# Performance work log

Hardware: AMD Instinct MI355X
Metric: run time of the kernel (lower is better)

Reference implementation:

```python
import jax, jax.numpy as jnp
import numpy as np

B, CL, QL, D = 32, 1024, 512, 256


def setup_inputs() -> dict:
    key = jax.random.key(0)
    ks = jax.random.split(key, 8)
    c = jax.random.normal(ks[0], (B, CL, D), jnp.float32)
    q = jax.random.normal(ks[1], (B, QL, D), jnp.float32)
    scale = 1.0 / np.sqrt(D)
    w_c = jax.random.normal(ks[2], (D,), jnp.float32) * scale
    b_c = jax.random.normal(ks[3], (), jnp.float32) * 0.01
    w_q = jax.random.normal(ks[4], (D,), jnp.float32) * scale
    b_q = jax.random.normal(ks[5], (), jnp.float32) * 0.01
    w_cq = jax.random.normal(ks[6], (D,), jnp.float32) * scale
    b_cq = jax.random.normal(ks[7], (), jnp.float32) * 0.01
    return {"c": c, "q": q, "w_c": w_c, "b_c": b_c, "w_q": w_q, "b_q": b_q,
            "w_cq": w_cq, "b_cq": b_cq}


def reference(c, q, w_c, b_c, w_q, b_q, w_cq, b_cq):
    # s[b,i,j] = w_c.c_i + w_q.q_j + w_cq.(c_i*q_j) + biases
    sc = c @ w_c + b_c                                   # (B, CL)
    sq = q @ w_q + b_q                                   # (B, QL)
    # The original per-j loop att_weight_cq(c * q_j) is a batched bilinear form.
    cq = jnp.einsum('bid,bjd,d->bij', c, q, w_cq) + b_cq  # (B, CL, QL)
    s = sc[:, :, None] + sq[:, None, :] + cq              # (B, CL, QL)
    a = jax.nn.softmax(s, axis=2)
    c2q_att = jnp.einsum('bij,bjd->bid', a, q)            # (B, CL, D)
    bvec = jax.nn.softmax(jnp.max(s, axis=2), axis=1)     # (B, CL)
    q2c = jnp.einsum('bi,bid->bd', bvec, c)               # (B, D)
    q2c_att = jnp.broadcast_to(q2c[:, None, :], c.shape)  # (B, CL, D)
    x = jnp.concatenate([c, c2q_att, c * c2q_att, c * q2c_att], axis=-1)
    return x
```

## Files before the change

### kernel.cpp

```cpp
#include <hip/hip_runtime.h>

#define B_  32
#define CL_ 1024
#define QL_ 512
#define D_  256

typedef _Float16 f16;
typedef __attribute__((ext_vector_type(2))) _Float16 f16x2;
typedef __attribute__((ext_vector_type(4))) _Float16 f16x4;
typedef __attribute__((ext_vector_type(8))) _Float16 f16x8;
typedef __attribute__((ext_vector_type(4))) float    f32x4;

__global__ __launch_bounds__(256) void k0_prep(const float* __restrict__ q,
                                               const float* __restrict__ w_q,
                                               f16* __restrict__ q_h,
                                               f16* __restrict__ qT_h,
                                               float* __restrict__ sqv) {
  __shared__ f16 q_l[64][258];
  int b = blockIdx.y, j0 = blockIdx.x * 64, tid = threadIdx.x;
  int r = tid >> 2, seg = tid & 3;
  const float* qrow = q   + ((size_t)(b * QL_ + j0 + r)) * D_ + seg * 64;
  f16*        qhrow = q_h + ((size_t)(b * QL_ + j0 + r)) * D_ + seg * 64;
  float dot = 0.f;
  #pragma unroll
  for (int u = 0; u < 16; ++u) {
    f32x4 v  = *(const f32x4*)(qrow + 4 * u);
    f32x4 wv = *(const f32x4*)(w_q + seg * 64 + 4 * u);
    f16x4 h;
    h[0] = (f16)v[0]; h[1] = (f16)v[1]; h[2] = (f16)v[2]; h[3] = (f16)v[3];
    *(f16x4*)(&q_l[r][seg * 64 + 4 * u]) = h;
    *(f16x4*)(qhrow + 4 * u) = h;
    dot += v[0]*wv[0] + v[1]*wv[1] + v[2]*wv[2] + v[3]*wv[3];
  }
  dot += __shfl_xor(dot, 1, 64);
  dot += __shfl_xor(dot, 2, 64);
  if (seg == 0) sqv[b * QL_ + j0 + r] = dot;
  __syncthreads();
  f16* qTb = qT_h + (size_t)b * D_ * QL_ + j0;
  #pragma unroll
  for (int s = 0; s < 32; ++s) {
    int e = tid + 256 * s;
    int d = e >> 5, j2 = (e & 31) * 2;
    f16x2 p;
    p[0] = q_l[j2][d];
    p[1] = q_l[j2 + 1][d];
    *(f16x2*)(qTb + (size_t)d * QL_ + j2) = p;
  }
}

__global__ __launch_bounds__(512, 4) void k1_fused(
    const float* __restrict__ c, const f16* __restrict__ q_h,
    const f16* __restrict__ qT_h, const float* __restrict__ sqv,
    const float* __restrict__ w_c, const float* __restrict__ w_cq,
    float* __restrict__ out, float* __restrict__ mrow)
{
  __shared__ alignas(16) char smem[73472];
  f16 (*cw_t)[264]  = (f16 (*)[264])(smem);
  f16 (*P_t)[520]   = (f16 (*)[520])(smem);
  float (*o_l)[260] = (float (*)[260])(smem);
  float* sqv_l = (float*)(smem + 66560);
  float* wcq_l = (float*)(smem + 68608);
  float* wc_l  = (float*)(smem + 69632);
  float* scv_l = (float*)(smem + 70656);
  float (*red)[64] = (float (*)[64])(smem + 70912);
  float* mf = (float*)(smem + 72960);
  float* lf = (float*)(smem + 73216);

  const int tid = threadIdx.x;
  const int w = tid >> 6, l = tid & 63, g = l >> 4, l15 = l & 15;
  const int lin = blockIdx.x, xcd = lin & 7, slot = lin >> 3;
  const int b  = xcd * 4 + (slot >> 4);
  const int i0 = (slot & 15) * 64;

  if (tid < 256) { wcq_l[tid] = w_cq[tid]; wc_l[tid] = w_c[tid]; }
  sqv_l[tid] = sqv[b * QL_ + tid];
  __syncthreads();

  {
    int row = tid >> 3, seg = tid & 7;
    const float* crow = c + (size_t)(b * CL_ + i0 + row) * D_ + seg * 32;
    float dot = 0.f;
    #pragma unroll
    for (int u = 0; u < 8; ++u) {
      f32x4 v  = *(const f32x4*)(crow + 4 * u);
      f32x4 wv = *(const f32x4*)(wcq_l + seg * 32 + 4 * u);
      f32x4 w2 = *(const f32x4*)(wc_l  + seg * 32 + 4 * u);
      f16x4 h;
      h[0] = (f16)(v[0]*wv[0]); h[1] = (f16)(v[1]*wv[1]);
      h[2] = (f16)(v[2]*wv[2]); h[3] = (f16)(v[3]*wv[3]);
      *(f16x4*)(&cw_t[row][seg * 32 + 4 * u]) = h;
      dot += v[0]*w2[0] + v[1]*w2[1] + v[2]*w2[2] + v[3]*w2[3];
    }
    dot += __shfl_xor(dot, 1, 64); dot += __shfl_xor(dot, 2, 64);
    dot += __shfl_xor(dot, 4, 64);
    if (seg == 0) scv_l[row] = dot;
  }
  __syncthreads();

  f32x4 acc[4][4];
  #pragma unroll
  for (int fi = 0; fi < 4; ++fi)
    #pragma unroll
    for (int fj = 0; fj < 4; ++fj)
      acc[fi][fj] = (f32x4){0.f,0.f,0.f,0.f};

  const f16* qb = q_h + (size_t)b * QL_ * D_ + (size_t)(64 * w + l15) * D_ + 8 * g;
  #pragma unroll
  for (int dk = 0; dk < 8; ++dk) {
    f16x8 av[4];
    #pragma unroll
    for (int fi = 0; fi < 4; ++fi)
      av[fi] = *(const f16x8*)(&cw_t[16 * fi + l15][dk * 32 + 8 * g]);
    #pragma unroll
    for (int fj = 0; fj < 4; ++fj) {
      f16x8 bf = *(const f16x8*)(qb + (size_t)(16 * fj) * D_ + dk * 32);
      #pragma unroll
      for (int fi = 0; fi < 4; ++fi)
        acc[fi][fj] = __builtin_amdgcn_mfma_f32_16x16x32_f16(av[fi], bf, acc[fi][fj], 0, 0, 0);
    }
  }

  #pragma unroll
  for (int fi = 0; fi < 4; ++fi) {
    #pragma unroll
    for (int r = 0; r < 4; ++r) {
      float mx = -1e30f;
      #pragma unroll
      for (int fj = 0; fj < 4; ++fj) {
        float v = acc[fi][fj][r] + sqv_l[64 * w + 16 * fj + l15];
        acc[fi][fj][r] = v;
        mx = fmaxf(mx, v);
      }
      mx = fmaxf(mx, __shfl_xor(mx, 1, 64));
      mx = fmaxf(mx, __shfl_xor(mx, 2, 64));
      mx = fmaxf(mx, __shfl_xor(mx, 4, 64));
      mx = fmaxf(mx, __shfl_xor(mx, 8, 64));
      if (l15 == 0) red[w][16 * fi + 4 * g + r] = mx;
    }
  }
  __syncthreads();
  if (tid < 64) {
    float m = red[0][tid];
    #pragma unroll
    for (int w2 = 1; w2 < 8; ++w2) m = fmaxf(m, red[w2][tid]);
    mf[tid] = m;
    mrow[b * CL_ + i0 + tid] = m + scv_l[tid];
  }
  __syncthreads();
  #pragma unroll
  for (int fi = 0; fi < 4; ++fi) {
    #pragma unroll
    for (int r = 0; r < 4; ++r) {
      float mv = mf[16 * fi + 4 * g + r];
      float s = 0.f;
      #pragma unroll
      for (int fj = 0; fj < 4; ++fj) {
        float p = __expf(acc[fi][fj][r] - mv);
        acc[fi][fj][r] = p;
        s += p;
      }
      s += __shfl_xor(s, 1, 64); s += __shfl_xor(s, 2, 64);
      s += __shfl_xor(s, 4, 64); s += __shfl_xor(s, 8, 64);
      if (l15 == 0) red[w][16 * fi + 4 * g + r] = s;
    }
  }
  __syncthreads();
  if (tid < 64) {
    float s = 0.f;
    #pragma unroll
    for (int w2 = 0; w2 < 8; ++w2) s += red[w2][tid];
    lf[tid] = 1.0f / s;
  }
  __syncthreads();

  #pragma unroll
  for (int fi = 0; fi < 4; ++fi) {
    #pragma unroll
    for (int r = 0; r < 4; ++r) {
      int row = 16 * fi + 4 * g + r;
      float inv = lf[row];
      #pragma unroll
      for (int fj = 0; fj < 4; ++fj)
        P_t[row][64 * w + 16 * fj + l15] = (f16)(acc[fi][fj][r] * inv);
    }
  }
  __syncthreads();

  f32x4 o[4][2];
  #pragma unroll
  for (int fi = 0; fi < 4; ++fi) { o[fi][0] = (f32x4){0.f,0.f,0.f,0.f}; o[fi][1] = o[fi][0]; }
  const f16* qTb = qT_h + (size_t)b * D_ * QL_ + (size_t)(32 * w + l15) * QL_ + 8 * g;
  #pragma unroll
  for (int jt = 0; jt < 16; ++jt) {
    f16x8 qf0 = *(const f16x8*)(qTb + jt * 32);
    f16x8 qf1 = *(const f16x8*)(qTb + 16 * QL_ + jt * 32);
    #pragma unroll
    for (int fi = 0; fi < 4; ++fi) {
      f16x8 pa = *(const f16x8*)(&P_t[16 * fi + l15][jt * 32 + 8 * g]);
      o[fi][0] = __builtin_amdgcn_mfma_f32_16x16x32_f16(pa, qf0, o[fi][0], 0, 0, 0);
      o[fi][1] = __builtin_amdgcn_mfma_f32_16x16x32_f16(pa, qf1, o[fi][1], 0, 0, 0);
    }
  }
  __syncthreads();

  #pragma unroll
  for (int fi = 0; fi < 4; ++fi)
    #pragma unroll
    for (int fd = 0; fd < 2; ++fd)
      #pragma unroll
      for (int r = 0; r < 4; ++r)
        o_l[16 * fi + 4 * g + r][32 * w + 16 * fd + l15] = o[fi][fd][r];
  __syncthreads();

  #pragma unroll
  for (int s = 0; s < 8; ++s) {
    int idx = tid + 512 * s;
    int row = idx >> 6, c4 = (idx & 63) * 4;
    size_t rowoff = (size_t)(b * CL_ + i0 + row);
    f32x4 c2q = *(const f32x4*)(&o_l[row][c4]);
    f32x4 cv  = *(const f32x4*)(c + rowoff * D_ + c4);
    f32x4 prod;
    prod[0] = cv[0]*c2q[0]; prod[1] = cv[1]*c2q[1];
    prod[2] = cv[2]*c2q[2]; prod[3] = cv[3]*c2q[3];
    float* ob = out + rowoff * (4 * D_) + c4;
    *(f32x4*)(ob)          = cv;
    *(f32x4*)(ob + D_)     = c2q;
    *(f32x4*)(ob + 2 * D_) = prod;
  }
}

__global__ __launch_bounds__(256) void k2a_bvec(const float* __restrict__ mrow,
                                                float* __restrict__ bvec) {
  __shared__ float red[256];
  int b = blockIdx.x, tid = threadIdx.x;
  f32x4 v = *(const f32x4*)(mrow + b * CL_ + tid * 4);
  float mx = fmaxf(fmaxf(v[0], v[1]), fmaxf(v[2], v[3]));
  red[tid] = mx;
  __syncthreads();
  for (int s = 128; s > 0; s >>= 1) {
    if (tid < s) red[tid] = fmaxf(red[tid], red[tid + s]);
    __syncthreads();
  }
  float gmx = red[0];
  __syncthreads();
  f32x4 e;
  e[0] = __expf(v[0] - gmx); e[1] = __expf(v[1] - gmx);
  e[2] = __expf(v[2] - gmx); e[3] = __expf(v[3] - gmx);
  red[tid] = e[0] + e[1] + e[2] + e[3];
  __syncthreads();
  for (int s = 128; s > 0; s >>= 1) {
    if (tid < s) red[tid] += red[tid + s];
    __syncthreads();
  }
  float inv = 1.0f / red[0];
  e[0] *= inv; e[1] *= inv; e[2] *= inv; e[3] *= inv;
  *(f32x4*)(bvec + b * CL_ + tid * 4) = e;
}

__global__ __launch_bounds__(256) void k2b_part(const float* __restrict__ c,
                                                const float* __restrict__ bvec,
                                                float* __restrict__ part) {
  __shared__ f32x4 pl[4][64];
  int ch = blockIdx.x, b = blockIdx.y, tid = threadIdx.x;
  int ro = tid >> 6, dl = tid & 63;
  const float* cb = c + ((size_t)b * CL_ + ch * 128) * D_;
  const float* bv = bvec + b * CL_ + ch * 128;
  f32x4 acc = (f32x4){0.f, 0.f, 0.f, 0.f};
  for (int i = ro; i < 128; i += 4) {
    float wgt = bv[i];
    f32x4 v = *(const f32x4*)(cb + (size_t)i * D_ + dl * 4);
    acc[0] += wgt * v[0]; acc[1] += wgt * v[1];
    acc[2] += wgt * v[2]; acc[3] += wgt * v[3];
  }
  pl[ro][dl] = acc;
  __syncthreads();
  if (tid < 64) {
    f32x4 s = (pl[0][tid] + pl[1][tid]) + (pl[2][tid] + pl[3][tid]);
    *(f32x4*)(part + ((size_t)(b * 8 + ch)) * D_ + tid * 4) = s;
  }
}

__global__ __launch_bounds__(256) void k2c_red(const float* __restrict__ part,
                                               float* __restrict__ q2c) {
  int b = blockIdx.x, d = threadIdx.x;
  float s = 0.f;
  #pragma unroll
  for (int ch = 0; ch < 8; ++ch) s += part[((size_t)(b * 8 + ch)) * D_ + d];
  q2c[b * D_ + d] = s;
}

__global__ __launch_bounds__(256) void k3_tail(const float* __restrict__ c,
                                               const float* __restrict__ q2c,
                                               float* __restrict__ out) {
  size_t idx = (size_t)blockIdx.x * 256 + threadIdx.x;
  int b   = (int)(idx >> 16);
  int rem = (int)(idx & 65535);
  int i = rem >> 6, d4 = (rem & 63) * 4;
  f32x4 cv = *(const f32x4*)(c + (size_t)(b * CL_ + i) * D_ + d4);
  f32x4 gv = *(const f32x4*)(q2c + b * D_ + d4);
  f32x4 r;
  r[0] = cv[0]*gv[0]; r[1] = cv[1]*gv[1]; r[2] = cv[2]*gv[2]; r[3] = cv[3]*gv[3];
  *(f32x4*)(out + (size_t)(b * CL_ + i) * (4 * D_) + 3 * D_ + d4) = r;
}

extern "C" void kernel_launch(void* const* d_in, const int* in_sizes, int n_in,
                              void* d_out, int out_size, void* d_ws, size_t ws_size,
                              hipStream_t stream) {
  const float* c    = (const float*)d_in[0];
  const float* q    = (const float*)d_in[1];
  const float* w_c  = (const float*)d_in[2];
  const float* w_q  = (const float*)d_in[4];
  const float* w_cq = (const float*)d_in[6];
  float* out = (float*)d_out;
  char* ws = (char*)d_ws;
  f16*   q_h  = (f16*)ws;
  f16*   qT_h = (f16*)(ws + 8388608);
  float* sqv  = (float*)(ws + 16777216);
  float* mrow = (float*)(ws + 16842752);
  float* bvec = (float*)(ws + 16973824);
  float* part = (float*)(ws + 17104896);
  float* q2c  = (float*)(ws + 17367040);

  hipLaunchKernelGGL(k0_prep,  dim3(8, 32),  dim3(256), 0, stream,
                     q, w_q, q_h, qT_h, sqv);
  hipLaunchKernelGGL(k1_fused, dim3(512),    dim3(512), 0, stream,
                     c, q_h, qT_h, sqv, w_c, w_cq, out, mrow);
  hipLaunchKernelGGL(k2a_bvec, dim3(32),     dim3(256), 0, stream, mrow, bvec);
  hipLaunchKernelGGL(k2b_part, dim3(8, 32),  dim3(256), 0, stream, c, bvec, part);
  hipLaunchKernelGGL(k2c_red,  dim3(32),     dim3(256), 0, stream, part, q2c);
  hipLaunchKernelGGL(k3_tail,  dim3(8192),   dim3(256), 0, stream, c, q2c, out);
}
```

Measured before the change: 101.2 us.

## Split fused attention kernel into scores, softmax and PV GEMM kernels

Replaces the single fused kernel with three kernels. The first computes the scores and writes them to a global f16 buffer. The second applies the row softmax in place and records row maxima. The third runs a finer-tiled PV GEMM with smaller blocks and writes the output slices. The intent is to raise occupancy and parallelism of the PV stage and to shorten the long fused kernel. In exchange it adds large global round-trips of the score matrix, extra launches, and f16 rounding of the scores before the softmax.

Result: slower. 146.1 us (+44.4%).

```diff
diff --git a/kernel.cpp b/kernel.cpp
--- a/kernel.cpp
+++ b/kernel.cpp
@@ -48,23 +48,18 @@
   }
 }
 
-__global__ __launch_bounds__(512, 4) void k1_fused(
+__global__ __launch_bounds__(512, 2) void kU_scores(
     const float* __restrict__ c, const f16* __restrict__ q_h,
-    const f16* __restrict__ qT_h, const float* __restrict__ sqv,
-    const float* __restrict__ w_c, const float* __restrict__ w_cq,
-    float* __restrict__ out, float* __restrict__ mrow)
+    const float* __restrict__ sqv, const float* __restrict__ w_c,
+    const float* __restrict__ w_cq, f16* __restrict__ Ug,
+    float* __restrict__ scv_ws)
 {
-  __shared__ alignas(16) char smem[73472];
-  f16 (*cw_t)[264]  = (f16 (*)[264])(smem);
-  f16 (*P_t)[520]   = (f16 (*)[520])(smem);
-  float (*o_l)[260] = (float (*)[260])(smem);
+  __shared__ alignas(16) char smem[71680];
+  f16 (*cw_t)[264] = (f16 (*)[264])(smem);
+  f16 (*U_t)[520]  = (f16 (*)[520])(smem);
   float* sqv_l = (float*)(smem + 66560);
   float* wcq_l = (float*)(smem + 68608);
   float* wc_l  = (float*)(smem + 69632);
-  float* scv_l = (float*)(smem + 70656);
-  float (*red)[64] = (float (*)[64])(smem + 70912);
-  float* mf = (float*)(smem + 72960);
-  float* lf = (float*)(smem + 73216);
 
   const int tid = threadIdx.x;
   const int w = tid >> 6, l = tid & 63, g = l >> 4, l15 = l & 15;
@@ -93,7 +88,7 @@
     }
     dot += __shfl_xor(dot, 1, 64); dot += __shfl_xor(dot, 2, 64);
     dot += __shfl_xor(dot, 4, 64);
-    if (seg == 0) scv_l[row] = dot;
+    if (seg == 0) scv_ws[b * CL_ + i0 + row] = dot;
   }
   __syncthreads();
 
@@ -119,110 +114,113 @@
         acc[fi][fj] = __builtin_amdgcn_mfma_f32_16x16x32_f16(av[fi], bf, acc[fi][fj], 0, 0, 0);
     }
   }
-
-  #pragma unroll
-  for (int fi = 0; fi < 4; ++fi) {
+  __syncthreads();
+
+  #pragma unroll
+  for (int fi = 0; fi < 4; ++fi)
     #pragma unroll
     for (int r = 0; r < 4; ++r) {
-      float mx = -1e30f;
+      int row = 16 * fi + 4 * g + r;
       #pragma unroll
       for (int fj = 0; fj < 4; ++fj) {
-        float v = acc[fi][fj][r] + sqv_l[64 * w + 16 * fj + l15];
-        acc[fi][fj][r] = v;
-        mx = fmaxf(mx, v);
+        int col = 64 * w + 16 * fj + l15;
+        U_t[row][col] = (f16)(acc[fi][fj][r] + sqv_l[col]);
       }
-      mx = fmaxf(mx, __shfl_xor(mx, 1, 64));
-      mx = fmaxf(mx, __shfl_xor(mx, 2, 64));
-      mx = fmaxf(mx, __shfl_xor(mx, 4, 64));
-      mx = fmaxf(mx, __shfl_xor(mx, 8, 64));
-      if (l15 == 0) red[w][16 * fi + 4 * g + r] = mx;
     }
-  }
-  __syncthreads();
-  if (tid < 64) {
-    float m = red[0][tid];
-    #pragma unroll
-    for (int w2 = 1; w2 < 8; ++w2) m = fmaxf(m, red[w2][tid]);
-    mf[tid] = m;
-    mrow[b * CL_ + i0 + tid] = m + scv_l[tid];
-  }
-  __syncthreads();
-  #pragma unroll
-  for (int fi = 0; fi < 4; ++fi) {
-    #pragma unroll
-    for (int r = 0; r < 4; ++r) {
-      float mv = mf[16 * fi + 4 * g + r];
-      float s = 0.f;
-      #pragma unroll
-      for (int fj = 0; fj < 4; ++fj) {
-        float p = __expf(acc[fi][fj][r] - mv);
-        acc[fi][fj][r] = p;
-        s += p;
-      }
-      s += __shfl_xor(s, 1, 64); s += __shfl_xor(s, 2, 64);
-      s += __shfl_xor(s, 4, 64); s += __shfl_xor(s, 8, 64);
-      if (l15 == 0) red[w][16 * fi + 4 * g + r] = s;
-    }
-  }
-  __syncthreads();
-  if (tid < 64) {
-    float s = 0.f;
-    #pragma unroll
-    for (int w2 = 0; w2 < 8; ++w2) s += red[w2][tid];
-    lf[tid] = 1.0f / s;
-  }
-  __syncthreads();
-
-  #pragma unroll
-  for (int fi = 0; fi < 4; ++fi) {
-    #pragma unroll
-    for (int r = 0; r < 4; ++r) {
-      int row = 16 * fi + 4 * g + r;
-      float inv = lf[row];
-      #pragma unroll
-      for (int fj = 0; fj < 4; ++fj)
-        P_t[row][64 * w + 16 * fj + l15] = (f16)(acc[fi][fj][r] * inv);
-    }
-  }
-  __syncthreads();
-
-  f32x4 o[4][2];
-  #pragma unroll
-  for (int fi = 0; fi < 4; ++fi) { o[fi][0] = (f32x4){0.f,0.f,0.f,0.f}; o[fi][1] = o[fi][0]; }
-  const f16* qTb = qT_h + (size_t)b * D_ * QL_ + (size_t)(32 * w + l15) * QL_ + 8 * g;
-  #pragma unroll
-  for (int jt = 0; jt < 16; ++jt) {
-    f16x8 qf0 = *(const f16x8*)(qTb + jt * 32);
-    f16x8 qf1 = *(const f16x8*)(qTb + 16 * QL_ + jt * 32);
-    #pragma unroll
-    for (int fi = 0; fi < 4; ++fi) {
-      f16x8 pa = *(const f16x8*)(&P_t[16 * fi + l15][jt * 32 + 8 * g]);
-      o[fi][0] = __builtin_amdgcn_mfma_f32_16x16x32_f16(pa, qf0, o[fi][0], 0, 0, 0);
-      o[fi][1] = __builtin_amdgcn_mfma_f32_16x16x32_f16(pa, qf1, o[fi][1], 0, 0, 0);
-    }
-  }
-  __syncthreads();
-
-  #pragma unroll
-  for (int fi = 0; fi < 4; ++fi)
+  __syncthreads();
+
+  f16* Ub = Ug + ((size_t)(b * CL_ + i0)) * QL_;
+  #pragma unroll
+  for (int s = 0; s < 8; ++s) {
+    int idx = tid + 512 * s;
+    int row = idx >> 6, col8 = (idx & 63) * 8;
+    *(f16x8*)(Ub + (size_t)row * QL_ + col8) = *(const f16x8*)(&U_t[row][col8]);
+  }
+}
+
+__global__ __launch_bounds__(256) void kSM_softmax(
+    f16* __restrict__ UPg, const float* __restrict__ scv_ws,
+    float* __restrict__ mrow)
+{
+  int gr   = blockIdx.x * 4 + (threadIdx.x >> 6);
+  int lane = threadIdx.x & 63;
+  f16* rp = UPg + (size_t)gr * QL_ + lane * 8;
+  f16x8 uv = *(const f16x8*)rp;
+  float u[8];
+  #pragma unroll
+  for (int k = 0; k < 8; ++k) u[k] = (float)uv[k];
+  float mx = u[0];
+  #pragma unroll
+  for (int k = 1; k < 8; ++k) mx = fmaxf(mx, u[k]);
+  #pragma unroll
+  for (int m = 1; m < 64; m <<= 1) mx = fmaxf(mx, __shfl_xor(mx, m, 64));
+  if (lane == 0) mrow[gr] = mx + scv_ws[gr];
+  float s = 0.f;
+  #pragma unroll
+  for (int k = 0; k < 8; ++k) { u[k] = __expf(u[k] - mx); s += u[k]; }
+  #pragma unroll
+  for (int m = 1; m < 64; m <<= 1) s += __shfl_xor(s, m, 64);
+  float inv = 1.0f / s;
+  f16x8 pv;
+  #pragma unroll
+  for (int k = 0; k < 8; ++k) pv[k] = (f16)(u[k] * inv);
+  *(f16x8*)rp = pv;
+}
+
+__global__ __launch_bounds__(256, 4) void kPV_gemm(
+    const float* __restrict__ c, const f16* __restrict__ Pg,
+    const f16* __restrict__ qT_h, float* __restrict__ out)
+{
+  __shared__ float o_l[64][68];
+  const int tid = threadIdx.x;
+  const int w = tid >> 6, l = tid & 63, g = l >> 4, l15 = l & 15;
+  const int lin = blockIdx.x, xcd = lin & 7, slot = lin >> 3;
+  const int b   = xcd * 4 + (slot >> 6);
+  const int rem = slot & 63;
+  const int i0 = (rem >> 2) * 64, d0 = (rem & 3) * 64;
+  const int wi = w >> 1, wd = w & 1;
+
+  const f16* a0p = Pg + ((size_t)(b * CL_ + i0 + 32 * wi + l15)) * QL_ + 8 * g;
+  const f16* a1p = a0p + 16 * QL_;
+  const f16* b0p = qT_h + (size_t)b * D_ * QL_
+                 + (size_t)(d0 + 32 * wd + l15) * QL_ + 8 * g;
+  const f16* b1p = b0p + 16 * QL_;
+
+  f32x4 acc[2][2];
+  acc[0][0] = (f32x4){0.f,0.f,0.f,0.f}; acc[0][1] = acc[0][0];
+  acc[1][0] = acc[0][0];                acc[1][1] = acc[0][0];
+  #pragma unroll
+  for (int kt = 0; kt < 16; ++kt) {
+    f16x8 a0 = *(const f16x8*)(a0p + kt * 32);
+    f16x8 a1 = *(const f16x8*)(a1p + kt * 32);
+    f16x8 b0 = *(const f16x8*)(b0p + kt * 32);
+    f16x8 b1 = *(const f16x8*)(b1p + kt * 32);
+    acc[0][0] = __builtin_amdgcn_mfma_f32_16x16x32_f16(a0, b0, acc[0][0], 0, 0, 0);
+    acc[0][1] = __builtin_amdgcn_mfma_f32_16x16x32_f16(a0, b1, acc[0][1], 0, 0, 0);
+    acc[1][0] = __builtin_amdgcn_mfma_f32_16x16x32_f16(a1, b0, acc[1][0], 0, 0, 0);
+    acc[1][1] = __builtin_amdgcn_mfma_f32_16x16x32_f16(a1, b1, acc[1][1], 0, 0, 0);
+  }
+
+  #pragma unroll
+  for (int fi = 0; fi < 2; ++fi)
     #pragma unroll
     for (int fd = 0; fd < 2; ++fd)
       #pragma unroll
       for (int r = 0; r < 4; ++r)
-        o_l[16 * fi + 4 * g + r][32 * w + 16 * fd + l15] = o[fi][fd][r];
-  __syncthreads();
-
-  #pragma unroll
-  for (int s = 0; s < 8; ++s) {
-    int idx = tid + 512 * s;
-    int row = idx >> 6, c4 = (idx & 63) * 4;
+        o_l[32 * wi + 16 * fi + 4 * g + r][32 * wd + 16 * fd + l15] = acc[fi][fd][r];
+  __syncthreads();
+
+  #pragma unroll
+  for (int s = 0; s < 4; ++s) {
+    int chunk = tid + 256 * s;
+    int row = chunk >> 4, col = (chunk & 15) * 4;
     size_t rowoff = (size_t)(b * CL_ + i0 + row);
-    f32x4 c2q = *(const f32x4*)(&o_l[row][c4]);
-    f32x4 cv  = *(const f32x4*)(c + rowoff * D_ + c4);
+    f32x4 c2q = *(const f32x4*)(&o_l[row][col]);
+    f32x4 cv  = *(const f32x4*)(c + rowoff * D_ + d0 + col);
     f32x4 prod;
     prod[0] = cv[0]*c2q[0]; prod[1] = cv[1]*c2q[1];
     prod[2] = cv[2]*c2q[2]; prod[3] = cv[3]*c2q[3];
-    float* ob = out + rowoff * (4 * D_) + c4;
+    float* ob = out + rowoff * (4 * D_) + d0 + col;
     *(f32x4*)(ob)          = cv;
     *(f32x4*)(ob + D_)     = c2q;
     *(f32x4*)(ob + 2 * D_) = prod;
@@ -313,20 +311,26 @@
   const float* w_cq = (const float*)d_in[6];
   float* out = (float*)d_out;
   char* ws = (char*)d_ws;
-  f16*   q_h  = (f16*)ws;
-  f16*   qT_h = (f16*)(ws + 8388608);
-  float* sqv  = (float*)(ws + 16777216);
-  float* mrow = (float*)(ws + 16842752);
-  float* bvec = (float*)(ws + 16973824);
-  float* part = (float*)(ws + 17104896);
-  float* q2c  = (float*)(ws + 17367040);
-
-  hipLaunchKernelGGL(k0_prep,  dim3(8, 32),  dim3(256), 0, stream,
+  f16*   q_h    = (f16*)ws;
+  f16*   qT_h   = (f16*)(ws + 8388608);
+  float* sqv    = (float*)(ws + 16777216);
+  float* mrow   = (float*)(ws + 16842752);
+  float* bvec   = (float*)(ws + 16973824);
+  float* part   = (float*)(ws + 17104896);
+  float* q2c    = (float*)(ws + 17367040);
+  float* scv_ws = (float*)(ws + 17399808);
+  f16*   UPg    = (f16*)(ws + 17530880);
+
+  hipLaunchKernelGGL(k0_prep,    dim3(8, 32),  dim3(256), 0, stream,
                      q, w_q, q_h, qT_h, sqv);
-  hipLaunchKernelGGL(k1_fused, dim3(512),    dim3(512), 0, stream,
-                     c, q_h, qT_h, sqv, w_c, w_cq, out, mrow);
-  hipLaunchKernelGGL(k2a_bvec, dim3(32),     dim3(256), 0, stream, mrow, bvec);
-  hipLaunchKernelGGL(k2b_part, dim3(8, 32),  dim3(256), 0, stream, c, bvec, part);
-  hipLaunchKernelGGL(k2c_red,  dim3(32),     dim3(256), 0, stream, part, q2c);
-  hipLaunchKernelGGL(k3_tail,  dim3(8192),   dim3(256), 0, stream, c, q2c, out);
-}
+  hipLaunchKernelGGL(kU_scores,  dim3(512),    dim3(512), 0, stream,
+                     c, q_h, sqv, w_c, w_cq, UPg, scv_ws);
+  hipLaunchKernelGGL(kSM_softmax,dim3(8192),   dim3(256), 0, stream,
+                     UPg, scv_ws, mrow);
+  hipLaunchKernelGGL(kPV_gemm,   dim3(2048),   dim3(256), 0, stream,
+                     c, UPg, qT_h, out);
+  hipLaunchKernelGGL(k2a_bvec,   dim3(32),     dim3(256), 0, stream, mrow, bvec);
+  hipLaunchKernelGGL(k2b_part,   dim3(8, 32),  dim3(256), 0, stream, c, bvec, part);
+  hipLaunchKernelGGL(k2c_red,    dim3(32),     dim3(256), 0, stream, part, q2c);
+  hipLaunchKernelGGL(k3_tail,    dim3(8192),   dim3(256), 0, stream, c, q2c, out);
+}
```

## Stage q and qT tiles through swizzled LDS for both GEMMs

Applied to the files above, without the earlier changes.

Replaces per-wave direct global loads of q and q-transpose fragments with cooperative block-wide loads into XOR-swizzled shared-memory tiles. The first GEMM is restructured into four j-chunks, and the second into four staged j-chunks. The goal is coalesced global reads and cheaper LDS-fed MFMA operands in place of strided 16-byte global loads. In exchange, LDS grows to about 136 KB, which cuts blocks per CU (the occupancy hint is dropped) and adds extra barriers per chunk.

New measurement: 178.6 us. 76.4% more time.

```diff
diff --git a/kernel.cpp b/kernel.cpp
--- a/kernel.cpp
+++ b/kernel.cpp
@@ -48,23 +48,25 @@
   }
 }
 
-__global__ __launch_bounds__(512, 4) void k1_fused(
+__global__ __launch_bounds__(512) void k1_fused(
     const float* __restrict__ c, const f16* __restrict__ q_h,
     const f16* __restrict__ qT_h, const float* __restrict__ sqv,
     const float* __restrict__ w_c, const float* __restrict__ w_cq,
     float* __restrict__ out, float* __restrict__ mrow)
 {
-  __shared__ alignas(16) char smem[73472];
+  __shared__ alignas(16) char smem[139008];
   f16 (*cw_t)[264]  = (f16 (*)[264])(smem);
+  char* qA          = smem + 34816;
   f16 (*P_t)[520]   = (f16 (*)[520])(smem);
+  char* qT          = smem + 66560;
   float (*o_l)[260] = (float (*)[260])(smem);
-  float* sqv_l = (float*)(smem + 66560);
-  float* wcq_l = (float*)(smem + 68608);
-  float* wc_l  = (float*)(smem + 69632);
-  float* scv_l = (float*)(smem + 70656);
-  float (*red)[64] = (float (*)[64])(smem + 70912);
-  float* mf = (float*)(smem + 72960);
-  float* lf = (float*)(smem + 73216);
+  float* sqv_l = (float*)(smem + 132096);
+  float* wcq_l = (float*)(smem + 134144);
+  float* wc_l  = (float*)(smem + 135168);
+  float* scv_l = (float*)(smem + 136192);
+  float (*red)[64] = (float (*)[64])(smem + 136448);
+  float* mf = (float*)(smem + 138496);
+  float* lf = (float*)(smem + 138752);
 
   const int tid = threadIdx.x;
   const int w = tid >> 6, l = tid & 63, g = l >> 4, l15 = l & 15;
@@ -95,29 +97,38 @@
     dot += __shfl_xor(dot, 4, 64);
     if (seg == 0) scv_l[row] = dot;
   }
-  __syncthreads();
 
   f32x4 acc[4][4];
   #pragma unroll
-  for (int fi = 0; fi < 4; ++fi)
-    #pragma unroll
-    for (int fj = 0; fj < 4; ++fj)
-      acc[fi][fj] = (f32x4){0.f,0.f,0.f,0.f};
-
-  const f16* qb = q_h + (size_t)b * QL_ * D_ + (size_t)(64 * w + l15) * D_ + 8 * g;
-  #pragma unroll
-  for (int dk = 0; dk < 8; ++dk) {
-    f16x8 av[4];
+  for (int jc = 0; jc < 4; ++jc)
     #pragma unroll
     for (int fi = 0; fi < 4; ++fi)
-      av[fi] = *(const f16x8*)(&cw_t[16 * fi + l15][dk * 32 + 8 * g]);
-    #pragma unroll
-    for (int fj = 0; fj < 4; ++fj) {
-      f16x8 bf = *(const f16x8*)(qb + (size_t)(16 * fj) * D_ + dk * 32);
-      #pragma unroll
-      for (int fi = 0; fi < 4; ++fi)
-        acc[fi][fj] = __builtin_amdgcn_mfma_f32_16x16x32_f16(av[fi], bf, acc[fi][fj], 0, 0, 0);
-    }
+      acc[jc][fi] = (f32x4){0.f,0.f,0.f,0.f};
+
+  const char* qhbC = (const char*)(q_h + (size_t)b * QL_ * D_);
+  const int jrow = 16 * w + l15;
+  const int jsw  = jrow & 7;
+  #pragma unroll 1
+  for (int jc = 0; jc < 4; ++jc) {
+    const char* src = qhbC + (size_t)jc * 65536;
+    #pragma unroll
+    for (int s = 0; s < 8; ++s) {
+      int idx = s * 512 + tid;
+      int row = idx >> 5, sl = idx & 31;
+      f32x4 v = *(const f32x4*)(src + (size_t)idx * 16);
+      *(f32x4*)(qA + row * 512 + ((sl ^ (row & 7)) << 4)) = v;
+    }
+    __syncthreads();
+    #pragma unroll
+    for (int dk = 0; dk < 8; ++dk) {
+      f16x8 bf = *(const f16x8*)(qA + jrow * 512 + (((dk * 4 + g) ^ jsw) << 4));
+      #pragma unroll
+      for (int fi = 0; fi < 4; ++fi) {
+        f16x8 av = *(const f16x8*)(&cw_t[16 * fi + l15][dk * 32 + 8 * g]);
+        acc[jc][fi] = __builtin_amdgcn_mfma_f32_16x16x32_f16(av, bf, acc[jc][fi], 0, 0, 0);
+      }
+    }
+    __syncthreads();
   }
 
   #pragma unroll
@@ -126,9 +137,9 @@
     for (int r = 0; r < 4; ++r) {
       float mx = -1e30f;
       #pragma unroll
-      for (int fj = 0; fj < 4; ++fj) {
-        float v = acc[fi][fj][r] + sqv_l[64 * w + 16 * fj + l15];
-        acc[fi][fj][r] = v;
+      for (int jc = 0; jc < 4; ++jc) {
+        float v = acc[jc][fi][r] + sqv_l[jc * 128 + jrow];
+        acc[jc][fi][r] = v;
         mx = fmaxf(mx, v);
       }
       mx = fmaxf(mx, __shfl_xor(mx, 1, 64));
@@ -154,9 +165,9 @@
       float mv = mf[16 * fi + 4 * g + r];
       float s = 0.f;
       #pragma unroll
-      for (int fj = 0; fj < 4; ++fj) {
-        float p = __expf(acc[fi][fj][r] - mv);
-        acc[fi][fj][r] = p;
+      for (int jc = 0; jc < 4; ++jc) {
+        float p = __expf(acc[jc][fi][r] - mv);
+        acc[jc][fi][r] = p;
         s += p;
       }
       s += __shfl_xor(s, 1, 64); s += __shfl_xor(s, 2, 64);
@@ -180,25 +191,38 @@
       int row = 16 * fi + 4 * g + r;
       float inv = lf[row];
       #pragma unroll
-      for (int fj = 0; fj < 4; ++fj)
-        P_t[row][64 * w + 16 * fj + l15] = (f16)(acc[fi][fj][r] * inv);
-    }
-  }
-  __syncthreads();
+      for (int jc = 0; jc < 4; ++jc)
+        P_t[row][jc * 128 + jrow] = (f16)(acc[jc][fi][r] * inv);
+    }
+  }
 
   f32x4 o[4][2];
   #pragma unroll
   for (int fi = 0; fi < 4; ++fi) { o[fi][0] = (f32x4){0.f,0.f,0.f,0.f}; o[fi][1] = o[fi][0]; }
-  const f16* qTb = qT_h + (size_t)b * D_ * QL_ + (size_t)(32 * w + l15) * QL_ + 8 * g;
-  #pragma unroll
-  for (int jt = 0; jt < 16; ++jt) {
-    f16x8 qf0 = *(const f16x8*)(qTb + jt * 32);
-    f16x8 qf1 = *(const f16x8*)(qTb + 16 * QL_ + jt * 32);
-    #pragma unroll
-    for (int fi = 0; fi < 4; ++fi) {
-      f16x8 pa = *(const f16x8*)(&P_t[16 * fi + l15][jt * 32 + 8 * g]);
-      o[fi][0] = __builtin_amdgcn_mfma_f32_16x16x32_f16(pa, qf0, o[fi][0], 0, 0, 0);
-      o[fi][1] = __builtin_amdgcn_mfma_f32_16x16x32_f16(pa, qf1, o[fi][1], 0, 0, 0);
+  const char* qTbC = (const char*)(qT_h + (size_t)b * D_ * QL_);
+  const int drow0 = 32 * w + l15, drow1 = drow0 + 16;
+  #pragma unroll 1
+  for (int jc = 0; jc < 4; ++jc) {
+    __syncthreads();
+    #pragma unroll
+    for (int s = 0; s < 8; ++s) {
+      int idx = s * 512 + tid;
+      int row = idx >> 4, sl = idx & 15;
+      f32x4 v = *(const f32x4*)(qTbC + (size_t)row * 1024 + jc * 256 + sl * 16);
+      *(f32x4*)(qT + row * 256 + ((sl ^ (row & 7)) << 4)) = v;
+    }
+    __syncthreads();
+    #pragma unroll
+    for (int jtl = 0; jtl < 4; ++jtl) {
+      f16x8 qf0 = *(const f16x8*)(qT + drow0 * 256 + (((jtl * 4 + g) ^ (drow0 & 7)) << 4));
+      f16x8 qf1 = *(const f16x8*)(qT + drow1 * 256 + (((jtl * 4 + g) ^ (drow1 & 7)) << 4));
+      int jt = jc * 4 + jtl;
+      #pragma unroll
+      for (int fi = 0; fi < 4; ++fi) {
+        f16x8 pa = *(const f16x8*)(&P_t[16 * fi + l15][jt * 32 + 8 * g]);
+        o[fi][0] = __builtin_amdgcn_mfma_f32_16x16x32_f16(pa, qf0, o[fi][0], 0, 0, 0);
+        o[fi][1] = __builtin_amdgcn_mfma_f32_16x16x32_f16(pa, qf1, o[fi][1], 0, 0, 0);
+      }
     }
   }
   __syncthreads();
```
